# Kernel optimization log

Measured on AMD Instinct MI355X. Metric: run time of the kernel, lower is better.

## Reference

```python
import jax, jax.numpy as jnp
import numpy as np

N = 50000
E = 800000
IN_DIM = 64          # 'in_dim'; ndata h has dim 2*in_dim, p has dim in_dim
EDGE_DIM = 32
OUT_DIM = 64
AVG_D_LOG = 2.8332   # avg_d['log'] = log(avg_degree + 1), avg_degree = 16
EPS_STD = 1e-5
EPS_BN = 1e-5


def setup_inputs() -> dict:
    key = jax.random.key(0)
    ks = jax.random.split(key, 16)
    def glorot(k, fan_in, fan_out):
        lim = np.sqrt(6.0 / (fan_in + fan_out)).astype(np.float32)
        return jax.random.uniform(k, (fan_in, fan_out), jnp.float32, -lim, lim)
    d_pre_h = 2 * 2 * IN_DIM + EDGE_DIM   # 288
    d_pre_p = 2 * IN_DIM + EDGE_DIM       # 160
    d_post_h = (4 * 3 + 2) * IN_DIM       # 896
    d_post_p = (4 * 3 + 1) * IN_DIM       # 832
    return {
        "h": jax.random.normal(ks[0], (N, 2 * IN_DIM), jnp.float32),
        "p": jax.random.normal(ks[1], (N, IN_DIM), jnp.float32),
        "e": jax.random.normal(ks[2], (E, EDGE_DIM), jnp.float32),
        "src": jax.random.randint(ks[3], (E,), 0, N, jnp.int32),
        "dst": jax.random.randint(ks[4], (E,), 0, N, jnp.int32),
        "snorm_n": jax.random.uniform(ks[5], (N, 1), jnp.float32, 0.05, 1.0),
        "W_pre_h": glorot(ks[6], d_pre_h, IN_DIM),
        "b_pre_h": jnp.zeros((IN_DIM,), jnp.float32),
        "W_pre_p": glorot(ks[7], d_pre_p, IN_DIM),
        "b_pre_p": jnp.zeros((IN_DIM,), jnp.float32),
        "W_post_h": glorot(ks[8], d_post_h, OUT_DIM),
        "b_post_h": jnp.zeros((OUT_DIM,), jnp.float32),
        "W_post_p": glorot(ks[9], d_post_p, OUT_DIM),
        "b_post_p": jnp.zeros((OUT_DIM,), jnp.float32),
        "bn_gamma": jnp.ones((OUT_DIM,), jnp.float32),
        "bn_beta": jnp.zeros((OUT_DIM,), jnp.float32),
    }


def _agg_scale(msg, dst, deg):
    # msg: [E, d] edge messages reduced at dst; PNA aggregators mean/max/min/std
    degc = jnp.maximum(deg, 1.0)
    s = jax.ops.segment_sum(msg, dst, num_segments=N)
    mean = s / degc[:, None]
    sq = jax.ops.segment_sum(msg * msg, dst, num_segments=N) / degc[:, None]
    var = jax.nn.relu(sq - mean * mean)
    std = jnp.sqrt(var + EPS_STD)
    has = (deg > 0)[:, None]
    mx = jnp.where(has, jax.ops.segment_max(msg, dst, num_segments=N), 0.0)
    mn = jnp.where(has, jax.ops.segment_min(msg, dst, num_segments=N), 0.0)
    agg = jnp.concatenate([mean, mx, mn, std], axis=1)  # [N, 4d]
    logd = jnp.where(deg > 0, jnp.log(deg + 1.0), 1.0)
    amp = (logd / AVG_D_LOG)[:, None]
    att = (AVG_D_LOG / logd)[:, None]
    # scalers: identity, amplification, attenuation -> [N, 12d]
    return jnp.concatenate([agg, agg * amp, agg * att], axis=1)


def reference(h, p, e, src, dst, snorm_n,
              W_pre_h, b_pre_h, W_pre_p, b_pre_p,
              W_post_h, b_post_h, W_post_p, b_post_p,
              bn_gamma, bn_beta):
    # pretrans (1-layer MLP == linear) on concatenated edge endpoint features
    z_h = jnp.concatenate([h[src], h[dst], e], axis=1)   # [E, 4*in+edge]
    z_p = jnp.concatenate([p[src], p[dst], e], axis=1)   # [E, 2*in+edge]
    e_for_h = z_h @ W_pre_h + b_pre_h                    # [E, in]
    e_for_p = z_p @ W_pre_p + b_pre_p                    # [E, in]

    deg = jax.ops.segment_sum(jnp.ones((E,), jnp.float32), dst, num_segments=N)
    agg_h = _agg_scale(e_for_h, dst, deg)                # [N, 12*in]
    agg_p = _agg_scale(e_for_p, dst, deg)                # [N, 12*in]

    h_cat = jnp.concatenate([h, agg_h], axis=1)          # [N, 14*in]
    p_cat = jnp.concatenate([p, agg_p], axis=1)          # [N, 13*in]
    h_out = h_cat @ W_post_h + b_post_h                  # [N, out]
    p_out = p_cat @ W_post_p + b_post_p                  # [N, out]

    # graph norm
    h_out = h_out * snorm_n
    # batch norm (training-mode batch statistics, biased variance)
    mu = jnp.mean(h_out, axis=0)
    var = jnp.mean((h_out - mu) ** 2, axis=0)
    h_out = (h_out - mu) / jnp.sqrt(var + EPS_BN) * bn_gamma + bn_beta
    # dropout = identity (eval / p=0)
    return h_out, p_out
```

## Files before the change

### kernel.cpp

```cpp
#include <hip/hip_runtime.h>
#include <hip/hip_bf16.h>
#include <hip/hip_fp16.h>


#define N_NODES 50000
#define N_EDGES 800000
#define NS 3200000
#define AVG_D_LOG 2.8332f

typedef unsigned short u16;
typedef unsigned int u32;
typedef __attribute__((ext_vector_type(8))) short short8;
typedef __attribute__((ext_vector_type(4))) float f32x4;

__device__ __forceinline__ float bflo(u32 u) { return __uint_as_float(u << 16); }
__device__ __forceinline__ float bfhi(u32 u) { return __uint_as_float(u & 0xffff0000u); }
__device__ __forceinline__ float bf2f(u16 u) { return __uint_as_float(((u32)u) << 16); }
__device__ __forceinline__ u16 f2bf(float x) {
  u32 u = __float_as_uint(x);
  return (u16)((u + 0x7fff + ((u >> 16) & 1)) >> 16);
}
__device__ __forceinline__ u16 f2h(float x) { return __half_as_ushort(__float2half(x)); }
__device__ __forceinline__ float h2f(u16 x) { return __half2float(__ushort_as_half(x)); }

__device__ __forceinline__ int is_bf(const void* gamma) {
  return ((const u32*)gamma)[0] == 0x3F803F80u ? 1 : 0;
}

__device__ __forceinline__ f32x4 mfma16(short8 a, short8 b, f32x4 c) {
  return __builtin_amdgcn_mfma_f32_16x16x32_bf16(a, b, c, 0, 0, 0);
}

__device__ __forceinline__ void load8(float z[8], const void* base, size_t off,
                                      int bf) {
  if (bf) {
    uint4 u = *(const uint4*)((const u16*)base + off);
    z[0] = bflo(u.x); z[1] = bfhi(u.x); z[2] = bflo(u.y); z[3] = bfhi(u.y);
    z[4] = bflo(u.z); z[5] = bfhi(u.z); z[6] = bflo(u.w); z[7] = bfhi(u.w);
  } else {
    const float* f = (const float*)base + off;
    float4 a = *(const float4*)f;
    float4 b = *(const float4*)(f + 4);
    z[0] = a.x; z[1] = a.y; z[2] = a.z; z[3] = a.w;
    z[4] = b.x; z[5] = b.y; z[6] = b.z; z[7] = b.w;
  }
}

__device__ __forceinline__ float load1(const void* base, size_t off, int bf) {
  return bf ? bf2f(((const u16*)base)[off]) : ((const float*)base)[off];
}

__global__ __launch_bounds__(256) void k_init(int* __restrict__ cnt,
                                              float* __restrict__ bnacc) {
  int i = blockIdx.x * 256 + threadIdx.x;
  if (i < N_NODES) cnt[i] = 0;
  else if (i < N_NODES + 128) bnacc[i - N_NODES] = 0.0f;
}

__global__ __launch_bounds__(256) void k_convert(
    const void* __restrict__ Wpreh, const void* __restrict__ Wprep,
    const void* __restrict__ Wposth, const void* __restrict__ Wpostp,
    const void* __restrict__ bpreh, const void* __restrict__ bprep,
    const void* __restrict__ bposth, const void* __restrict__ bpostp,
    const void* __restrict__ gamma, float* __restrict__ bias,
    u16* __restrict__ frag) {
  int i = blockIdx.x * 256 + threadIdx.x;
  if (i >= 256 + 139264) return;
  int bf = is_bf(gamma);
  if (i < 256) {
    const void* s = (i < 64) ? bpreh : (i < 128) ? bprep : (i < 192) ? bposth : bpostp;
    bias[i] = load1(s, i & 63, bf);
    return;
  }
  int g = i - 256;
  const void* W; int fidx, rowoff;
  if (g < 8192)        { W = Wpreh;  fidx = g;          rowoff = 0; }
  else if (g < 16384)  { W = Wpreh;  fidx = g - 8192;   rowoff = 128; }
  else if (g < 20480)  { W = Wprep;  fidx = g - 16384;  rowoff = 0; }
  else if (g < 24576)  { W = Wprep;  fidx = g - 20480;  rowoff = 64; }
  else if (g < 81920)  { W = Wposth; fidx = g - 24576;  rowoff = 0; }
  else if (g < 135168) { W = Wpostp; fidx = g - 81920;  rowoff = 0; }
  else if (g < 137216) { W = Wpreh;  fidx = g - 135168; rowoff = 256; }
  else                 { W = Wprep;  fidx = g - 137216; rowoff = 128; }
  int f = fidx;
  int kc = f >> 11, nt = (f >> 9) & 3, lane = (f >> 3) & 63, j = f & 7;
  int k = kc * 32 + (lane >> 4) * 8 + j;
  int n = nt * 16 + (lane & 15);
  frag[g] = f2bf(load1(W, (size_t)(rowoff + k) * 64 + n, bf));
}

__global__ __launch_bounds__(256) void k_hist(const int* __restrict__ dst,
                                              int* __restrict__ cnt) {
  int i = blockIdx.x * 256 + threadIdx.x;
  if (i < N_EDGES) atomicAdd(cnt + dst[i], 1);
}

__global__ __launch_bounds__(1024) void k_scan1(const int* __restrict__ cnt,
                                                int* __restrict__ offs,
                                                int* __restrict__ bsum) {
  __shared__ int buf[1024];
  int t = threadIdx.x;
  int i = blockIdx.x * 1024 + t;
  int v = (i < N_NODES) ? cnt[i] : 0;
  buf[t] = v;
  __syncthreads();
#pragma unroll
  for (int d = 1; d < 1024; d <<= 1) {
    int x = (t >= d) ? buf[t - d] : 0;
    __syncthreads();
    buf[t] += x;
    __syncthreads();
  }
  if (i < N_NODES) offs[i] = buf[t] - v;
  if (t == 1023) bsum[blockIdx.x] = buf[1023];
}
__global__ void k_scan2(const int* __restrict__ bsum, int* __restrict__ boff,
                        int* __restrict__ offs, int nb) {
  if (threadIdx.x == 0 && blockIdx.x == 0) {
    int run = 0;
    for (int b = 0; b < nb; ++b) { boff[b] = run; run += bsum[b]; }
    offs[N_NODES] = run;
  }
}
__global__ __launch_bounds__(256) void k_scan3(int* __restrict__ offs,
                                               const int* __restrict__ boff,
                                               int* __restrict__ cnt) {
  int i = blockIdx.x * 256 + threadIdx.x;
  if (i < N_NODES) {
    int v = offs[i] + boff[i >> 10];
    offs[i] = v;
    cnt[i] = v;
  }
}

__global__ __launch_bounds__(256) void k_order(const int* __restrict__ src,
                                               const int* __restrict__ dst,
                                               int* __restrict__ cnt,
                                               int2* __restrict__ epack) {
  int i = blockIdx.x * 256 + threadIdx.x;
  if (i < N_EDGES) {
    int pos = atomicAdd(cnt + dst[i], 1);
    epack[pos] = make_int2(i, src[i]);
  }
}

__global__ __launch_bounds__(256) void k_uproj(
    const void* __restrict__ h, const void* __restrict__ p,
    const float* __restrict__ bias, const u16* __restrict__ frag,
    const void* __restrict__ gamma, u16* __restrict__ Uhs,
    u16* __restrict__ Uhd, u16* __restrict__ Ups, u16* __restrict__ Upd) {
  int wid = (blockIdx.x * 256 + threadIdx.x) >> 6;
  int lane = threadIdx.x & 63;
  if (wid >= 12500) return;
  int part = wid / 3125;
  int node0 = (wid % 3125) * 16;
  int bf = is_bf(gamma);
  const void* feat = (part < 2) ? h : p;
  int pitch = (part < 2) ? 128 : 64;
  int kcn = (part < 2) ? 4 : 2;
  const u16* bfr = frag + (part == 0 ? 0 : part == 1 ? 8192 : part == 2 ? 16384 : 20480);
  u16* U = part == 0 ? Uhs : part == 1 ? Uhd : part == 2 ? Ups : Upd;
  int m = lane & 15, quad = lane >> 4;
  f32x4 acc[4];
#pragma unroll
  for (int nt = 0; nt < 4; ++nt) acc[nt] = (f32x4){0.f, 0.f, 0.f, 0.f};
#pragma unroll
  for (int kc = 0; kc < 4; ++kc) {
    if (kc >= kcn) break;
    float z[8];
    load8(z, feat, (size_t)(node0 + m) * pitch + kc * 32 + quad * 8, bf);
    short8 a;
#pragma unroll
    for (int q = 0; q < 8; ++q) a[q] = (short)f2bf(z[q]);
#pragma unroll
    for (int nt = 0; nt < 4; ++nt) {
      short8 b = *(const short8*)(bfr + (size_t)((kc * 4 + nt) * 64 + lane) * 8);
      acc[nt] = mfma16(a, b, acc[nt]);
    }
  }
  const float* bv = (part == 1) ? bias : (part == 3) ? bias + 64 : nullptr;
#pragma unroll
  for (int r = 0; r < 4; ++r) {
    int node = node0 + quad * 4 + r;
#pragma unroll
    for (int nt = 0; nt < 4; ++nt) {
      int col = nt * 16 + m;
      float v = acc[nt][r] + (bv ? bv[col] : 0.f);
      U[(size_t)node * 64 + col] = f2h(v);
    }
  }
}

template <int BF>
__global__ __launch_bounds__(256, 3) void k_aggf(
    const void* __restrict__ e, const int2* __restrict__ epack,
    const int* __restrict__ offs, const u16* __restrict__ Uhs,
    const u16* __restrict__ Uhd, const u16* __restrict__ Ups,
    const u16* __restrict__ Upd, const u16* __restrict__ Wfh,
    const u16* __restrict__ Wfp, const void* __restrict__ gamma,
    u16* __restrict__ Ah, u16* __restrict__ Ap, float* __restrict__ degf) {
  if (is_bf(gamma) != BF) return;
  int n = blockIdx.x * 4 + (threadIdx.x >> 6);
  int lane = threadIdx.x & 63;
  if (n >= N_NODES) return;
  int m = lane & 15, quad = lane >> 4;
  int s = offs[n], epos = offs[n + 1];
  int deg = epos - s;

  short8 bh[4], bp[4];
#pragma unroll
  for (int nt = 0; nt < 4; ++nt) {
    bh[nt] = *(const short8*)(Wfh + (size_t)(nt * 64 + lane) * 8);
    bp[nt] = *(const short8*)(Wfp + (size_t)(nt * 64 + lane) * 8);
  }
  float uhd[4], upd[4];
#pragma unroll
  for (int nt = 0; nt < 4; ++nt) {
    uhd[nt] = h2f(Uhd[(size_t)n * 64 + nt * 16 + m]);
    upd[nt] = h2f(Upd[(size_t)n * 64 + nt * 16 + m]);
  }
  float hsum[4], hsq[4], hmx[4], hmn[4], psum[4], psq[4], pmx[4], pmn[4];
#pragma unroll
  for (int nt = 0; nt < 4; ++nt) {
    hsum[nt] = hsq[nt] = psum[nt] = psq[nt] = 0.f;
    hmx[nt] = pmx[nt] = -3.4e38f;
    hmn[nt] = pmn[nt] = 3.4e38f;
  }

  for (int c0 = 0; c0 < deg; c0 += 16) {
    int im = s + c0 + m; im = im < epos ? im : epos - 1;
    int eid = epack[im].x;
    int sce0, sce1, sce2, sce3;
    {
      int b0 = s + c0 + quad * 4;
      int i0 = b0 < epos ? b0 : epos - 1;
      int i1 = b0 + 1 < epos ? b0 + 1 : epos - 1;
      int i2 = b0 + 2 < epos ? b0 + 2 : epos - 1;
      int i3 = b0 + 3 < epos ? b0 + 3 : epos - 1;
      sce0 = epack[i0].y; sce1 = epack[i1].y;
      sce2 = epack[i2].y; sce3 = epack[i3].y;
    }
    float z[8];
    load8(z, e, (size_t)eid * 32 + quad * 8, BF);
    short8 a;
#pragma unroll
    for (int q = 0; q < 8; ++q) a[q] = (short)f2bf(z[q]);

    {
      f32x4 acc[4];
#pragma unroll
      for (int nt = 0; nt < 4; ++nt)
        acc[nt] = mfma16(a, bh[nt], (f32x4){0.f, 0.f, 0.f, 0.f});
      float us[4][4];
#pragma unroll
      for (int nt = 0; nt < 4; ++nt) {
        us[0][nt] = h2f(Uhs[(size_t)sce0 * 64 + nt * 16 + m]);
        us[1][nt] = h2f(Uhs[(size_t)sce1 * 64 + nt * 16 + m]);
        us[2][nt] = h2f(Uhs[(size_t)sce2 * 64 + nt * 16 + m]);
        us[3][nt] = h2f(Uhs[(size_t)sce3 * 64 + nt * 16 + m]);
      }
#pragma unroll
      for (int r = 0; r < 4; ++r) {
        bool valid = (c0 + quad * 4 + r) < deg;
#pragma unroll
        for (int nt = 0; nt < 4; ++nt) {
          float v = acc[nt][r] + uhd[nt] + us[r][nt];
          float vv = valid ? v : 0.f;
          hsum[nt] += vv;
          hsq[nt] = fmaf(vv, vv, hsq[nt]);
          hmx[nt] = valid ? fmaxf(hmx[nt], v) : hmx[nt];
          hmn[nt] = valid ? fminf(hmn[nt], v) : hmn[nt];
        }
      }
    }
    {
      f32x4 acc[4];
#pragma unroll
      for (int nt = 0; nt < 4; ++nt)
        acc[nt] = mfma16(a, bp[nt], (f32x4){0.f, 0.f, 0.f, 0.f});
      float us[4][4];
#pragma unroll
      for (int nt = 0; nt < 4; ++nt) {
        us[0][nt] = h2f(Ups[(size_t)sce0 * 64 + nt * 16 + m]);
        us[1][nt] = h2f(Ups[(size_t)sce1 * 64 + nt * 16 + m]);
        us[2][nt] = h2f(Ups[(size_t)sce2 * 64 + nt * 16 + m]);
        us[3][nt] = h2f(Ups[(size_t)sce3 * 64 + nt * 16 + m]);
      }
#pragma unroll
      for (int r = 0; r < 4; ++r) {
        bool valid = (c0 + quad * 4 + r) < deg;
#pragma unroll
        for (int nt = 0; nt < 4; ++nt) {
          float v = acc[nt][r] + upd[nt] + us[r][nt];
          float vv = valid ? v : 0.f;
          psum[nt] += vv;
          psq[nt] = fmaf(vv, vv, psq[nt]);
          pmx[nt] = valid ? fmaxf(pmx[nt], v) : pmx[nt];
          pmn[nt] = valid ? fminf(pmn[nt], v) : pmn[nt];
        }
      }
    }
  }

  float dv = (float)deg;
  bool has = deg > 0;
  float inv = has ? 1.f / dv : 1.f;
  if (lane == 0) degf[n] = dv;

#pragma unroll
  for (int nt = 0; nt < 4; ++nt) {
    hsum[nt] += __shfl_xor(hsum[nt], 16); hsum[nt] += __shfl_xor(hsum[nt], 32);
    hsq[nt] += __shfl_xor(hsq[nt], 16);   hsq[nt] += __shfl_xor(hsq[nt], 32);
    hmx[nt] = fmaxf(hmx[nt], __shfl_xor(hmx[nt], 16));
    hmx[nt] = fmaxf(hmx[nt], __shfl_xor(hmx[nt], 32));
    hmn[nt] = fminf(hmn[nt], __shfl_xor(hmn[nt], 16));
    hmn[nt] = fminf(hmn[nt], __shfl_xor(hmn[nt], 32));
    psum[nt] += __shfl_xor(psum[nt], 16); psum[nt] += __shfl_xor(psum[nt], 32);
    psq[nt] += __shfl_xor(psq[nt], 16);   psq[nt] += __shfl_xor(psq[nt], 32);
    pmx[nt] = fmaxf(pmx[nt], __shfl_xor(pmx[nt], 16));
    pmx[nt] = fmaxf(pmx[nt], __shfl_xor(pmx[nt], 32));
    pmn[nt] = fminf(pmn[nt], __shfl_xor(pmn[nt], 16));
    pmn[nt] = fminf(pmn[nt], __shfl_xor(pmn[nt], 32));
  }

#pragma unroll
  for (int nt = 0; nt < 4; ++nt) {
    {
      float mean = hsum[nt] * inv;
      float var = fmaf(-mean, mean, hsq[nt] * inv);
      var = var > 0.f ? var : 0.f;
      float sd = sqrtf(var + 1e-5f);
      float v1 = has ? hmx[nt] : 0.f;
      float v2 = has ? hmn[nt] : 0.f;
      float o = quad == 0 ? mean : quad == 1 ? v1 : quad == 2 ? v2 : sd;
      Ah[(size_t)n * 256 + quad * 64 + nt * 16 + m] = f2bf(o);
    }
    {
      float mean = psum[nt] * inv;
      float var = fmaf(-mean, mean, psq[nt] * inv);
      var = var > 0.f ? var : 0.f;
      float sd = sqrtf(var + 1e-5f);
      float v1 = has ? pmx[nt] : 0.f;
      float v2 = has ? pmn[nt] : 0.f;
      float o = quad == 0 ? mean : quad == 1 ? v1 : quad == 2 ? v2 : sd;
      Ap[(size_t)n * 256 + quad * 64 + nt * 16 + m] = f2bf(o);
    }
  }
}

__global__ __launch_bounds__(256) void k_node(
    const void* __restrict__ h, const void* __restrict__ p,
    const u16* __restrict__ Ah, const u16* __restrict__ Ap,
    const void* __restrict__ snorm, const float* __restrict__ degf,
    const u16* __restrict__ BfH, const u16* __restrict__ BfP,
    const float* __restrict__ biasH, const float* __restrict__ biasP,
    const void* __restrict__ gamma, float* __restrict__ outh,
    float* __restrict__ outp) {
  int w = (blockIdx.x * 256 + threadIdx.x) >> 6;
  int lane = threadIdx.x & 63;
  if (w >= N_NODES / 16) return;
  int bf = is_bf(gamma);
  int m = lane & 15, quad = lane >> 4;
  int node0 = w * 16;

  float ampr[4], attr[4];
#pragma unroll
  for (int r = 0; r < 4; ++r) {
    float dv = degf[node0 + quad * 4 + r];
    float logd = (dv > 0.5f) ? logf(dv + 1.f) : 1.f;
    ampr[r] = logd * (1.f / AVG_D_LOG);
    attr[r] = AVG_D_LOG / logd;
  }

  f32x4 accB[4], accA[4], accT[4];
#pragma unroll
  for (int nt = 0; nt < 4; ++nt) {
    accB[nt] = (f32x4){0.f, 0.f, 0.f, 0.f};
    accA[nt] = (f32x4){0.f, 0.f, 0.f, 0.f};
    accT[nt] = (f32x4){0.f, 0.f, 0.f, 0.f};
  }
#pragma unroll 2
  for (int kc = 0; kc < 12; ++kc) {
    short8 a;
    if (kc < 4) {
      float z[8];
      load8(z, h, (size_t)(node0 + m) * 128 + kc * 32 + quad * 8, bf);
#pragma unroll
      for (int q = 0; q < 8; ++q) a[q] = (short)f2bf(z[q]);
    } else {
      a = *(const short8*)(Ah + (size_t)(node0 + m) * 256 + (kc - 4) * 32 + quad * 8);
    }
#pragma unroll
    for (int nt = 0; nt < 4; ++nt)
      accB[nt] = mfma16(a, *(const short8*)(BfH + (size_t)((kc * 4 + nt) * 64 + lane) * 8), accB[nt]);
    if (kc >= 4) {
      int kk = kc - 4;
#pragma unroll
      for (int nt = 0; nt < 4; ++nt)
        accA[nt] = mfma16(a, *(const short8*)(BfH + 24576 + (size_t)((kk * 4 + nt) * 64 + lane) * 8), accA[nt]);
#pragma unroll
      for (int nt = 0; nt < 4; ++nt)
        accT[nt] = mfma16(a, *(const short8*)(BfH + 40960 + (size_t)((kk * 4 + nt) * 64 + lane) * 8), accT[nt]);
    }
  }
  float bH[4];
#pragma unroll
  for (int nt = 0; nt < 4; ++nt) bH[nt] = biasH[nt * 16 + m];
#pragma unroll
  for (int r = 0; r < 4; ++r) {
    int node = node0 + quad * 4 + r;
    float sn = load1(snorm, node, bf);
#pragma unroll
    for (int nt = 0; nt < 4; ++nt) {
      float v = accB[nt][r] + ampr[r] * accA[nt][r] + attr[r] * accT[nt][r] + bH[nt];
      outh[(size_t)node * 64 + nt * 16 + m] = v * sn;
    }
  }

#pragma unroll
  for (int nt = 0; nt < 4; ++nt) {
    accB[nt] = (f32x4){0.f, 0.f, 0.f, 0.f};
    accA[nt] = (f32x4){0.f, 0.f, 0.f, 0.f};
    accT[nt] = (f32x4){0.f, 0.f, 0.f, 0.f};
  }
#pragma unroll 2
  for (int kc = 0; kc < 10; ++kc) {
    short8 a;
    if (kc < 2) {
      float z[8];
      load8(z, p, (size_t)(node0 + m) * 64 + kc * 32 + quad * 8, bf);
#pragma unroll
      for (int q = 0; q < 8; ++q) a[q] = (short)f2bf(z[q]);
    } else {
      a = *(const short8*)(Ap + (size_t)(node0 + m) * 256 + (kc - 2) * 32 + quad * 8);
    }
#pragma unroll
    for (int nt = 0; nt < 4; ++nt)
      accB[nt] = mfma16(a, *(const short8*)(BfP + (size_t)((kc * 4 + nt) * 64 + lane) * 8), accB[nt]);
    if (kc >= 2) {
      int kk = kc - 2;
#pragma unroll
      for (int nt = 0; nt < 4; ++nt)
        accA[nt] = mfma16(a, *(const short8*)(BfP + 20480 + (size_t)((kk * 4 + nt) * 64 + lane) * 8), accA[nt]);
#pragma unroll
      for (int nt = 0; nt < 4; ++nt)
        accT[nt] = mfma16(a, *(const short8*)(BfP + 36864 + (size_t)((kk * 4 + nt) * 64 + lane) * 8), accT[nt]);
    }
  }
  float bP[4];
#pragma unroll
  for (int nt = 0; nt < 4; ++nt) bP[nt] = biasP[nt * 16 + m];
#pragma unroll
  for (int r = 0; r < 4; ++r) {
    int node = node0 + quad * 4 + r;
#pragma unroll
    for (int nt = 0; nt < 4; ++nt) {
      float v = accB[nt][r] + ampr[r] * accA[nt][r] + attr[r] * accT[nt][r] + bP[nt];
      outp[(size_t)node * 64 + nt * 16 + m] = v;
    }
  }
}

__global__ __launch_bounds__(256) void k_bnstats(const float* __restrict__ hpre,
                                                 float* __restrict__ bnacc) {
  int j = threadIdx.x & 63;
  float s = 0.0f, q = 0.0f;
  for (int n = blockIdx.x * 4 + (threadIdx.x >> 6); n < N_NODES;
       n += gridDim.x * 4) {
    float x = hpre[(size_t)n * 64 + j];
    s += x; q += x * x;
  }
  __shared__ float ls[256], lq[256];
  ls[threadIdx.x] = s; lq[threadIdx.x] = q;
  __syncthreads();
  if (threadIdx.x < 64) {
    s = ls[threadIdx.x] + ls[threadIdx.x + 64] + ls[threadIdx.x + 128] + ls[threadIdx.x + 192];
    q = lq[threadIdx.x] + lq[threadIdx.x + 64] + lq[threadIdx.x + 128] + lq[threadIdx.x + 192];
    atomicAdd(bnacc + threadIdx.x, s);
    atomicAdd(bnacc + 64 + threadIdx.x, q);
  }
}

__global__ __launch_bounds__(256) void k_bnapply(
    float* __restrict__ outh, const float* __restrict__ bnacc,
    const void* __restrict__ gamma, const void* __restrict__ beta) {
  int i = blockIdx.x * 256 + threadIdx.x;
  if (i >= NS) return;
  int bf = is_bf(gamma);
  int j = i & 63;
  const float invN = 1.0f / (float)N_NODES;
  float mu = bnacc[j] * invN;
  float var = fmaf(-mu, mu, bnacc[64 + j] * invN);
  var = var > 0.0f ? var : 0.0f;
  float sc = load1(gamma, j, bf) * rsqrtf(var + 1e-5f);
  float sh = load1(beta, j, bf) - mu * sc;
  outh[i] = fmaf(outh[i], sc, sh);
}

extern "C" void kernel_launch(void* const* d_in, const int* in_sizes, int n_in,
                              void* d_out, int out_size, void* d_ws,
                              size_t ws_size, hipStream_t stream) {
  const void* h = d_in[0];
  const void* p = d_in[1];
  const void* e = d_in[2];
  const int* src = (const int*)d_in[3];
  const int* dst = (const int*)d_in[4];
  const void* snorm = d_in[5];
  const void* Wpreh = d_in[6];
  const void* bpreh = d_in[7];
  const void* Wprep = d_in[8];
  const void* bprep = d_in[9];
  const void* Wposth = d_in[10];
  const void* bposth = d_in[11];
  const void* Wpostp = d_in[12];
  const void* bpostp = d_in[13];
  const void* gamma = d_in[14];
  const void* beta = d_in[15];

  float* ws = (float*)d_ws;
  u16* Uhs = (u16*)ws;
  u16* Uhd = Uhs + 3200000;
  u16* Ups = Uhd + 3200000;
  u16* Upd = Ups + 3200000;
  u16* Ah = (u16*)(ws + 6400000L);
  u16* Ap = (u16*)(ws + 12800000L);
  int2* epack = (int2*)(ws + 19200000L);
  int* cnt = (int*)(ws + 20800016L);
  int* offs = (int*)(ws + 20850016L);
  float* degf = ws + 20900020L;
  int* bsum = (int*)(ws + 20950020L);
  int* boff = (int*)(ws + 20950084L);
  float* bnacc = ws + 20950148L;
  float* bias = ws + 20950276L;
  u16* frag = (u16*)(ws + 20950532L);

  u16* fragPostH = frag + 24576;
  u16* fragPostP = frag + 81920;
  u16* fragWehF = frag + 135168;
  u16* fragWepF = frag + 137216;

  float* outh = (float*)d_out;
  float* outp = outh + (size_t)NS;

  int bfh = -1;
  if (in_sizes && n_in >= 16) {
    if (in_sizes[0] == 25600000) bfh = 0;
    else if (in_sizes[0] == 12800000) bfh = 1;
  }

  k_init<<<(N_NODES + 128 + 255) / 256, 256, 0, stream>>>(cnt, bnacc);
  k_convert<<<(256 + 139264 + 255) / 256, 256, 0, stream>>>(
      Wpreh, Wprep, Wposth, Wpostp, bpreh, bprep, bposth, bpostp, gamma, bias,
      frag);
  k_hist<<<(N_EDGES + 255) / 256, 256, 0, stream>>>(dst, cnt);
  const int NB = (N_NODES + 1023) / 1024;
  k_scan1<<<NB, 1024, 0, stream>>>(cnt, offs, bsum);
  k_scan2<<<1, 64, 0, stream>>>(bsum, boff, offs, NB);
  k_scan3<<<(N_NODES + 255) / 256, 256, 0, stream>>>(offs, boff, cnt);
  k_order<<<(N_EDGES + 255) / 256, 256, 0, stream>>>(src, dst, cnt, epack);
  k_uproj<<<(12500 + 3) / 4, 256, 0, stream>>>(h, p, bias, frag, gamma, Uhs,
                                               Uhd, Ups, Upd);
  if (bfh != 1)
    k_aggf<0><<<(N_NODES + 3) / 4, 256, 0, stream>>>(
        e, epack, offs, Uhs, Uhd, Ups, Upd, fragWehF, fragWepF, gamma, Ah, Ap,
        degf);
  if (bfh != 0)
    k_aggf<1><<<(N_NODES + 3) / 4, 256, 0, stream>>>(
        e, epack, offs, Uhs, Uhd, Ups, Upd, fragWehF, fragWepF, gamma, Ah, Ap,
        degf);
  k_node<<<(N_NODES / 16 + 3) / 4, 256, 0, stream>>>(
      h, p, Ah, Ap, snorm, degf, fragPostH, fragPostP, bias + 128, bias + 192,
      gamma, outh, outp);
  k_bnstats<<<256, 256, 0, stream>>>(outh, bnacc);
  k_bnapply<<<(NS + 255) / 256, 256, 0, stream>>>(outh, bnacc, gamma, beta);
}
```

Measured before the change: 517.1 us.

## Interleave h/p node projections and hoist dst term out of edge aggregation loop

The k_uproj outputs are stored interleaved, with the h and p half-precision values for a column packed into one 32-bit word. The aggregation kernel now does one gather per source node instead of two separate half loads. The destination-node projection is constant within a segment, so it is added once after the reduction to mean, max and min rather than per edge. Max and min no longer mask padded edges, because the clamped indices repeat a valid edge. The change also raises the occupancy hint to 4 and replaces the init kernel with two hipMemsetAsync calls. It trades slightly different rounding order for fewer loads and ALU ops in the edge loop.

Result: no change. 513.6 us (-0.7%).

```diff
diff --git a/kernel.cpp b/kernel.cpp
--- a/kernel.cpp
+++ b/kernel.cpp
@@ -22,6 +22,8 @@
 }
 __device__ __forceinline__ u16 f2h(float x) { return __half_as_ushort(__float2half(x)); }
 __device__ __forceinline__ float h2f(u16 x) { return __half2float(__ushort_as_half(x)); }
+__device__ __forceinline__ float hlo(u32 u) { return __half2float(__ushort_as_half((u16)(u & 0xffffu))); }
+__device__ __forceinline__ float hhi(u32 u) { return __half2float(__ushort_as_half((u16)(u >> 16))); }
 
 __device__ __forceinline__ int is_bf(const void* gamma) {
   return ((const u32*)gamma)[0] == 0x3F803F80u ? 1 : 0;
@@ -48,13 +50,6 @@
 
 __device__ __forceinline__ float load1(const void* base, size_t off, int bf) {
   return bf ? bf2f(((const u16*)base)[off]) : ((const float*)base)[off];
-}
-
-__global__ __launch_bounds__(256) void k_init(int* __restrict__ cnt,
-                                              float* __restrict__ bnacc) {
-  int i = blockIdx.x * 256 + threadIdx.x;
-  if (i < N_NODES) cnt[i] = 0;
-  else if (i < N_NODES + 128) bnacc[i - N_NODES] = 0.0f;
 }
 
 __global__ __launch_bounds__(256) void k_convert(
@@ -147,8 +142,8 @@
 __global__ __launch_bounds__(256) void k_uproj(
     const void* __restrict__ h, const void* __restrict__ p,
     const float* __restrict__ bias, const u16* __restrict__ frag,
-    const void* __restrict__ gamma, u16* __restrict__ Uhs,
-    u16* __restrict__ Uhd, u16* __restrict__ Ups, u16* __restrict__ Upd) {
+    const void* __restrict__ gamma, u16* __restrict__ Usrc,
+    u16* __restrict__ Udst) {
   int wid = (blockIdx.x * 256 + threadIdx.x) >> 6;
   int lane = threadIdx.x & 63;
   if (wid >= 12500) return;
@@ -159,7 +154,8 @@
   int pitch = (part < 2) ? 128 : 64;
   int kcn = (part < 2) ? 4 : 2;
   const u16* bfr = frag + (part == 0 ? 0 : part == 1 ? 8192 : part == 2 ? 16384 : 20480);
-  u16* U = part == 0 ? Uhs : part == 1 ? Uhd : part == 2 ? Ups : Upd;
+  u16* U = (part & 1) ? Udst : Usrc;
+  int tw = part >> 1;
   int m = lane & 15, quad = lane >> 4;
   f32x4 acc[4];
 #pragma unroll
@@ -186,17 +182,16 @@
     for (int nt = 0; nt < 4; ++nt) {
       int col = nt * 16 + m;
       float v = acc[nt][r] + (bv ? bv[col] : 0.f);
-      U[(size_t)node * 64 + col] = f2h(v);
+      U[(size_t)node * 128 + col * 2 + tw] = f2h(v);
     }
   }
 }
 
 template <int BF>
-__global__ __launch_bounds__(256, 3) void k_aggf(
+__global__ __launch_bounds__(256, 4) void k_aggf(
     const void* __restrict__ e, const int2* __restrict__ epack,
-    const int* __restrict__ offs, const u16* __restrict__ Uhs,
-    const u16* __restrict__ Uhd, const u16* __restrict__ Ups,
-    const u16* __restrict__ Upd, const u16* __restrict__ Wfh,
+    const int* __restrict__ offs, const u32* __restrict__ Us32,
+    const u32* __restrict__ Ud32, const u16* __restrict__ Wfh,
     const u16* __restrict__ Wfp, const void* __restrict__ gamma,
     u16* __restrict__ Ah, u16* __restrict__ Ap, float* __restrict__ degf) {
   if (is_bf(gamma) != BF) return;
@@ -216,8 +211,8 @@
   float uhd[4], upd[4];
 #pragma unroll
   for (int nt = 0; nt < 4; ++nt) {
-    uhd[nt] = h2f(Uhd[(size_t)n * 64 + nt * 16 + m]);
-    upd[nt] = h2f(Upd[(size_t)n * 64 + nt * 16 + m]);
+    u32 u = Ud32[(size_t)n * 64 + nt * 16 + m];
+    uhd[nt] = hlo(u); upd[nt] = hhi(u);
   }
   float hsum[4], hsq[4], hmx[4], hmn[4], psum[4], psq[4], pmx[4], pmn[4];
 #pragma unroll
@@ -230,47 +225,48 @@
   for (int c0 = 0; c0 < deg; c0 += 16) {
     int im = s + c0 + m; im = im < epos ? im : epos - 1;
     int eid = epack[im].x;
-    int sce0, sce1, sce2, sce3;
-    {
-      int b0 = s + c0 + quad * 4;
-      int i0 = b0 < epos ? b0 : epos - 1;
-      int i1 = b0 + 1 < epos ? b0 + 1 : epos - 1;
-      int i2 = b0 + 2 < epos ? b0 + 2 : epos - 1;
-      int i3 = b0 + 3 < epos ? b0 + 3 : epos - 1;
-      sce0 = epack[i0].y; sce1 = epack[i1].y;
-      sce2 = epack[i2].y; sce3 = epack[i3].y;
+    int b0 = s + c0 + quad * 4;
+    int i0 = b0 < epos ? b0 : epos - 1;
+    int i1 = b0 + 1 < epos ? b0 + 1 : epos - 1;
+    int i2 = b0 + 2 < epos ? b0 + 2 : epos - 1;
+    int i3 = b0 + 3 < epos ? b0 + 3 : epos - 1;
+    int sce0 = epack[i0].y, sce1 = epack[i1].y;
+    int sce2 = epack[i2].y, sce3 = epack[i3].y;
+    u32 usv0[4], usv1[4], usv2[4], usv3[4];
+#pragma unroll
+    for (int nt = 0; nt < 4; ++nt) {
+      usv0[nt] = Us32[(size_t)sce0 * 64 + nt * 16 + m];
+      usv1[nt] = Us32[(size_t)sce1 * 64 + nt * 16 + m];
+      usv2[nt] = Us32[(size_t)sce2 * 64 + nt * 16 + m];
+      usv3[nt] = Us32[(size_t)sce3 * 64 + nt * 16 + m];
     }
     float z[8];
     load8(z, e, (size_t)eid * 32 + quad * 8, BF);
     short8 a;
 #pragma unroll
     for (int q = 0; q < 8; ++q) a[q] = (short)f2bf(z[q]);
+    bool v0 = (c0 + quad * 4 + 0) < deg;
+    bool v1 = (c0 + quad * 4 + 1) < deg;
+    bool v2 = (c0 + quad * 4 + 2) < deg;
+    bool v3 = (c0 + quad * 4 + 3) < deg;
 
     {
       f32x4 acc[4];
 #pragma unroll
       for (int nt = 0; nt < 4; ++nt)
         acc[nt] = mfma16(a, bh[nt], (f32x4){0.f, 0.f, 0.f, 0.f});
-      float us[4][4];
 #pragma unroll
       for (int nt = 0; nt < 4; ++nt) {
-        us[0][nt] = h2f(Uhs[(size_t)sce0 * 64 + nt * 16 + m]);
-        us[1][nt] = h2f(Uhs[(size_t)sce1 * 64 + nt * 16 + m]);
-        us[2][nt] = h2f(Uhs[(size_t)sce2 * 64 + nt * 16 + m]);
-        us[3][nt] = h2f(Uhs[(size_t)sce3 * 64 + nt * 16 + m]);
-      }
-#pragma unroll
-      for (int r = 0; r < 4; ++r) {
-        bool valid = (c0 + quad * 4 + r) < deg;
-#pragma unroll
-        for (int nt = 0; nt < 4; ++nt) {
-          float v = acc[nt][r] + uhd[nt] + us[r][nt];
-          float vv = valid ? v : 0.f;
-          hsum[nt] += vv;
-          hsq[nt] = fmaf(vv, vv, hsq[nt]);
-          hmx[nt] = valid ? fmaxf(hmx[nt], v) : hmx[nt];
-          hmn[nt] = valid ? fminf(hmn[nt], v) : hmn[nt];
-        }
+        float w0 = acc[nt][0] + hlo(usv0[nt]);
+        float w1 = acc[nt][1] + hlo(usv1[nt]);
+        float w2 = acc[nt][2] + hlo(usv2[nt]);
+        float w3 = acc[nt][3] + hlo(usv3[nt]);
+        hmx[nt] = fmaxf(fmaxf(hmx[nt], w0), fmaxf(fmaxf(w1, w2), w3));
+        hmn[nt] = fminf(fminf(hmn[nt], w0), fminf(fminf(w1, w2), w3));
+        float z0 = v0 ? w0 : 0.f, z1 = v1 ? w1 : 0.f;
+        float z2 = v2 ? w2 : 0.f, z3 = v3 ? w3 : 0.f;
+        hsum[nt] += (z0 + z1) + (z2 + z3);
+        hsq[nt] = fmaf(z0, z0, fmaf(z1, z1, fmaf(z2, z2, fmaf(z3, z3, hsq[nt]))));
       }
     }
     {
@@ -278,26 +274,18 @@
 #pragma unroll
       for (int nt = 0; nt < 4; ++nt)
         acc[nt] = mfma16(a, bp[nt], (f32x4){0.f, 0.f, 0.f, 0.f});
-      float us[4][4];
 #pragma unroll
       for (int nt = 0; nt < 4; ++nt) {
-        us[0][nt] = h2f(Ups[(size_t)sce0 * 64 + nt * 16 + m]);
-        us[1][nt] = h2f(Ups[(size_t)sce1 * 64 + nt * 16 + m]);
-        us[2][nt] = h2f(Ups[(size_t)sce2 * 64 + nt * 16 + m]);
-        us[3][nt] = h2f(Ups[(size_t)sce3 * 64 + nt * 16 + m]);
-      }
-#pragma unroll
-      for (int r = 0; r < 4; ++r) {
-        bool valid = (c0 + quad * 4 + r) < deg;
-#pragma unroll
-        for (int nt = 0; nt < 4; ++nt) {
-          float v = acc[nt][r] + upd[nt] + us[r][nt];
-          float vv = valid ? v : 0.f;
-          psum[nt] += vv;
-          psq[nt] = fmaf(vv, vv, psq[nt]);
-          pmx[nt] = valid ? fmaxf(pmx[nt], v) : pmx[nt];
-          pmn[nt] = valid ? fminf(pmn[nt], v) : pmn[nt];
-        }
+        float w0 = acc[nt][0] + hhi(usv0[nt]);
+        float w1 = acc[nt][1] + hhi(usv1[nt]);
+        float w2 = acc[nt][2] + hhi(usv2[nt]);
+        float w3 = acc[nt][3] + hhi(usv3[nt]);
+        pmx[nt] = fmaxf(fmaxf(pmx[nt], w0), fmaxf(fmaxf(w1, w2), w3));
+        pmn[nt] = fminf(fminf(pmn[nt], w0), fminf(fminf(w1, w2), w3));
+        float z0 = v0 ? w0 : 0.f, z1 = v1 ? w1 : 0.f;
+        float z2 = v2 ? w2 : 0.f, z3 = v3 ? w3 : 0.f;
+        psum[nt] += (z0 + z1) + (z2 + z3);
+        psq[nt] = fmaf(z0, z0, fmaf(z1, z1, fmaf(z2, z2, fmaf(z3, z3, psq[nt]))));
       }
     }
   }
@@ -326,23 +314,23 @@
 #pragma unroll
   for (int nt = 0; nt < 4; ++nt) {
     {
-      float mean = hsum[nt] * inv;
-      float var = fmaf(-mean, mean, hsq[nt] * inv);
+      float mean_w = hsum[nt] * inv;
+      float var = fmaf(-mean_w, mean_w, hsq[nt] * inv);
       var = var > 0.f ? var : 0.f;
       float sd = sqrtf(var + 1e-5f);
-      float v1 = has ? hmx[nt] : 0.f;
-      float v2 = has ? hmn[nt] : 0.f;
-      float o = quad == 0 ? mean : quad == 1 ? v1 : quad == 2 ? v2 : sd;
+      float o = quad == 0 ? (has ? mean_w + uhd[nt] : 0.f)
+              : quad == 1 ? (has ? hmx[nt] + uhd[nt] : 0.f)
+              : quad == 2 ? (has ? hmn[nt] + uhd[nt] : 0.f) : sd;
       Ah[(size_t)n * 256 + quad * 64 + nt * 16 + m] = f2bf(o);
     }
     {
-      float mean = psum[nt] * inv;
-      float var = fmaf(-mean, mean, psq[nt] * inv);
+      float mean_w = psum[nt] * inv;
+      float var = fmaf(-mean_w, mean_w, psq[nt] * inv);
       var = var > 0.f ? var : 0.f;
       float sd = sqrtf(var + 1e-5f);
-      float v1 = has ? pmx[nt] : 0.f;
-      float v2 = has ? pmn[nt] : 0.f;
-      float o = quad == 0 ? mean : quad == 1 ? v1 : quad == 2 ? v2 : sd;
+      float o = quad == 0 ? (has ? mean_w + upd[nt] : 0.f)
+              : quad == 1 ? (has ? pmx[nt] + upd[nt] : 0.f)
+              : quad == 2 ? (has ? pmn[nt] + upd[nt] : 0.f) : sd;
       Ap[(size_t)n * 256 + quad * 64 + nt * 16 + m] = f2bf(o);
     }
   }
@@ -518,10 +506,8 @@
   const void* beta = d_in[15];
 
   float* ws = (float*)d_ws;
-  u16* Uhs = (u16*)ws;
-  u16* Uhd = Uhs + 3200000;
-  u16* Ups = Uhd + 3200000;
-  u16* Upd = Ups + 3200000;
+  u16* Usrc = (u16*)ws;
+  u16* Udst = (u16*)(ws + 3200000L);
   u16* Ah = (u16*)(ws + 6400000L);
   u16* Ap = (u16*)(ws + 12800000L);
   int2* epack = (int2*)(ws + 19200000L);
@@ -548,7 +534,8 @@
     else if (in_sizes[0] == 12800000) bfh = 1;
   }
 
-  k_init<<<(N_NODES + 128 + 255) / 256, 256, 0, stream>>>(cnt, bnacc);
+  hipMemsetAsync(cnt, 0, N_NODES * sizeof(int), stream);
+  hipMemsetAsync(bnacc, 0, 128 * sizeof(float), stream);
   k_convert<<<(256 + 139264 + 255) / 256, 256, 0, stream>>>(
       Wpreh, Wprep, Wposth, Wpostp, bpreh, bprep, bposth, bpostp, gamma, bias,
       frag);
@@ -558,16 +545,16 @@
   k_scan2<<<1, 64, 0, stream>>>(bsum, boff, offs, NB);
   k_scan3<<<(N_NODES + 255) / 256, 256, 0, stream>>>(offs, boff, cnt);
   k_order<<<(N_EDGES + 255) / 256, 256, 0, stream>>>(src, dst, cnt, epack);
-  k_uproj<<<(12500 + 3) / 4, 256, 0, stream>>>(h, p, bias, frag, gamma, Uhs,
-                                               Uhd, Ups, Upd);
+  k_uproj<<<(12500 + 3) / 4, 256, 0, stream>>>(h, p, bias, frag, gamma, Usrc,
+                                               Udst);
   if (bfh != 1)
     k_aggf<0><<<(N_NODES + 3) / 4, 256, 0, stream>>>(
-        e, epack, offs, Uhs, Uhd, Ups, Upd, fragWehF, fragWepF, gamma, Ah, Ap,
-        degf);
+        e, epack, offs, (const u32*)Usrc, (const u32*)Udst, fragWehF, fragWepF,
+        gamma, Ah, Ap, degf);
   if (bfh != 0)
     k_aggf<1><<<(N_NODES + 3) / 4, 256, 0, stream>>>(
-        e, epack, offs, Uhs, Uhd, Ups, Upd, fragWehF, fragWepF, gamma, Ah, Ap,
-        degf);
+        e, epack, offs, (const u32*)Usrc, (const u32*)Udst, fragWehF, fragWepF,
+        gamma, Ah, Ap, degf);
   k_node<<<(N_NODES / 16 + 3) / 4, 256, 0, stream>>>(
       h, p, Ah, Ap, snorm, degf, fragPostH, fragPostP, bias + 128, bias + 192,
       gamma, outh, outp);
```
